# Performance work log

Measured on AMD Instinct MI355X. Metric: run time of the kernel, lower is better.

## Reference

```python
import jax, jax.numpy as jnp
import numpy as np

D = 256
B, S, N = 4, 512, 4


def setup_inputs() -> dict:
    key = jax.random.key(0)
    ks = jax.random.split(key, 24)
    d, dq = D, D // 4
    std = 0.02
    inp = {
        'x':   jax.random.normal(ks[0], (B, S, N, d), jnp.float32),
        'Wq':  jax.random.normal(ks[1], (d, d), jnp.float32) * std,
        'Wk':  jax.random.normal(ks[2], (d, d), jnp.float32) * std,
        'Wv':  jax.random.normal(ks[3], (d, d), jnp.float32) * std,
        'Wg1': jax.random.normal(ks[4], (d, d), jnp.float32) * std,
        'bg1': jnp.zeros((d,), jnp.float32),
        'Wg2': jax.random.normal(ks[5], (d, d), jnp.float32) * std,
        'bg2': jnp.zeros((d,), jnp.float32),
        'We1': jax.random.normal(ks[6], (d, dq), jnp.float32) * std,
        'be1': jnp.zeros((dq,), jnp.float32),
        'We2': jax.random.normal(ks[7], (dq, 1), jnp.float32) * std,
        'be2': jnp.zeros((1,), jnp.float32),
        'Wa1': jax.random.normal(ks[8], (d, dq), jnp.float32) * std,
        'ba1': jnp.zeros((dq,), jnp.float32),
        'Wa2': jax.random.normal(ks[9], (dq, 1), jnp.float32) * std,
        'ba2': jnp.zeros((1,), jnp.float32),
        'Wo':  jax.random.normal(ks[10], (d, d), jnp.float32) * std,
        'bo':  jnp.zeros((d,), jnp.float32),
        'gamma': jnp.ones((d,), jnp.float32),
        'beta':  jnp.zeros((d,), jnp.float32),
    }
    return inp


def reference(x, Wq, Wk, Wv, Wg1, bg1, Wg2, bg2, We1, be1, We2, be2,
              Wa1, ba1, Wa2, ba2, Wo, bo, gamma, beta):
    b, s, n, f = x.shape
    xf = x.reshape(b * n, s, f)  # matches torch .view on contiguous x
    residual = xf

    q = xf @ Wq                                    # [bn, s, d]
    k = xf @ Wk
    v = xf @ Wv
    v_hat = jax.nn.silu(v @ Wg1 + bg1) @ Wg2 + bg2  # value_generator
    eta = jax.nn.sigmoid(jax.nn.silu(xf @ We1 + be1) @ We2 + be2) * 0.1 + 0.01   # [bn, s, 1]
    alpha = jax.nn.sigmoid(jax.nn.silu(xf @ Wa1 + ba1) @ Wa2 + ba2) * 0.5 + 0.5  # [bn, s, 1]

    # F.normalize(k, dim=-1): eps = 1e-12
    kn = k / jnp.maximum(jnp.linalg.norm(k, axis=-1, keepdims=True), 1e-12)

    M0 = jnp.zeros((b * n, f, f), x.dtype)

    def step(M, inp):
        q_t, k_t, v_t, e_t, a_t = inp  # [bn,d],[bn,d],[bn,d],[bn,1],[bn,1]
        out_t = jnp.einsum('bij,bj->bi', M, q_t)
        Mk = jnp.einsum('bij,bj->bi', M, k_t)
        e = e_t[:, :, None]  # [bn,1,1]
        a = a_t[:, :, None]
        # delta rule: M <- a*M - e*(Mk k^T) + e*(v k^T)
        M_new = a * M + e * ((v_t - Mk)[:, :, None] * k_t[:, None, :])
        return M_new, out_t

    seq = (jnp.swapaxes(q, 0, 1), jnp.swapaxes(kn, 0, 1), jnp.swapaxes(v_hat, 0, 1),
           jnp.swapaxes(eta, 0, 1), jnp.swapaxes(alpha, 0, 1))
    M, outs = jax.lax.scan(step, M0, seq)
    out = jnp.swapaxes(outs, 0, 1)  # [bn, s, d]

    y = out @ Wo + bo + residual  # dropout is identity in eval/reference
    mu = jnp.mean(y, axis=-1, keepdims=True)
    var = jnp.var(y, axis=-1, keepdims=True)
    y = (y - mu) / jnp.sqrt(var + 1e-5) * gamma + beta
    return y.reshape(b, s, n, f), M
```

## Files before the change

### kernel.cpp

```cpp
#include <hip/hip_runtime.h>

#define F_ 256
#define S_ 512
#define NH_ 16
#define CCH 32
#define NCH (S_/CCH)
#define KSTR 264
#define KTSTR 36
#define TSTR 40
#define PSTR 17

typedef __attribute__((ext_vector_type(8))) short short8_t;
typedef __attribute__((ext_vector_type(4))) float f32x4;

__device__ __forceinline__ float sigmoid_f(float x) { return 1.0f / (1.0f + __expf(-x)); }

__device__ __forceinline__ ushort f2bf(float x) {
  uint u = __float_as_uint(x);
  u += 0x7FFFu + ((u >> 16) & 1u);
  return (ushort)(u >> 16);
}
__device__ __forceinline__ float bf2f(ushort u) {
  return __uint_as_float((uint)u << 16);
}

template<int CTRL>
__device__ __forceinline__ float dpp_add(float x) {
  int y = __builtin_amdgcn_update_dpp(0, __float_as_int(x), CTRL, 0xf, 0xf, true);
  return x + __int_as_float(y);
}
__device__ __forceinline__ float red8(float x) {
  x = dpp_add<0xB1>(x);
  x = dpp_add<0x4E>(x);
  x = dpp_add<0x141>(x);
  return x;
}

__global__ __launch_bounds__(256) void wconv_k(
    const float* __restrict__ Wq, const float* __restrict__ Wk,
    const float* __restrict__ Wv, const float* __restrict__ Wg1,
    const float* __restrict__ Wg2, const float* __restrict__ Wo,
    const float* __restrict__ We1, const float* __restrict__ Wa1,
    const float* __restrict__ be1, const float* __restrict__ ba1,
    const float* __restrict__ x,
    ushort* __restrict__ Wt, float* __restrict__ beas,
    ushort* __restrict__ xb)
{
  const int blk = blockIdx.x, tid = threadIdx.x;
  if (blk >= 105) {
    const size_t base = (size_t)(blk - 105) * 16384;
    #pragma unroll
    for (int p = 0; p < 16; ++p) {
      const size_t o = base + (size_t)(((p << 8) + tid) << 2);
      const float4 v = *(const float4*)&x[o];
      ushort4 h4;
      h4.x = f2bf(v.x); h4.y = f2bf(v.y); h4.z = f2bf(v.z); h4.w = f2bf(v.w);
      *(ushort4*)&xb[o] = h4;
    }
    return;
  }
  if (blk == 104) {
    if (tid < 64) beas[tid] = be1[tid];
    else if (tid < 128) beas[tid] = ba1[tid - 64];
    return;
  }
  __shared__ float tile[64][65];
  const float* src; int N, k0, n0; size_t dstbase;
  if (blk < 96) {
    const int w = blk >> 4, tl = blk & 15;
    const float* ws_[6] = {Wq, Wk, Wv, Wg1, Wg2, Wo};
    const size_t dstb[6] = {0, 65536, 131072, 229376, 294912, 360448};
    src = ws_[w]; N = 256;
    k0 = (tl >> 2) * 64; n0 = (tl & 3) * 64;
    dstbase = dstb[w];
  } else {
    const int w = (blk - 96) >> 2, tl = (blk - 96) & 3;
    src = w ? Wa1 : We1; N = 64;
    k0 = tl * 64; n0 = 0;
    dstbase = w ? 212992 : 196608;
  }
  #pragma unroll
  for (int p = 0; p < 4; ++p) {
    const int idx = (p << 8) + tid;
    const int r = idx >> 4, c4 = (idx & 15) << 2;
    if (c4 < N) {
      const float4 v = *(const float4*)&src[(size_t)(k0 + r) * N + n0 + c4];
      tile[r][c4 + 0] = v.x; tile[r][c4 + 1] = v.y;
      tile[r][c4 + 2] = v.z; tile[r][c4 + 3] = v.w;
    }
  }
  __syncthreads();
  #pragma unroll
  for (int p = 0; p < 4; ++p) {
    const int idx = (p << 8) + tid;
    const int nl = idx >> 4, kc = (idx & 15) << 2;
    if (nl < ((blk < 96) ? 64 : 64) && (n0 + nl) < ((blk < 96) ? 256 : 64)) {
      ushort4 o;
      o.x = f2bf(tile[kc + 0][nl]); o.y = f2bf(tile[kc + 1][nl]);
      o.z = f2bf(tile[kc + 2][nl]); o.w = f2bf(tile[kc + 3][nl]);
      *(ushort4*)&Wt[dstbase + (size_t)(n0 + nl) * 256 + k0 + kc] = o;
    }
  }
}

__global__ __launch_bounds__(256) void qkve_k(
    const ushort* __restrict__ A, const ushort* __restrict__ Wt,
    const float* __restrict__ beas,
    ushort* __restrict__ qb, float* __restrict__ kf,
    ushort* __restrict__ vb, float* __restrict__ sesa)
{
  __shared__ ushort As[2][64 * 72];
  __shared__ ushort Ws[2][64 * 72];
  const int tid = threadIdx.x;
  const int wv = tid >> 6, l = tid & 63;
  const int ln = l & 15, hi = l >> 4, hi4 = hi << 2, hi8 = hi << 3;
  const int wr = wv >> 1, wc = wv & 1;
  const int row0 = blockIdx.y * 64, col0 = blockIdx.x * 64;
  const int r_ = tid >> 3, c8_ = (tid & 7) << 3;

  short8_t pA[2], pB[2];
  auto loadT = [&](int k0) {
    pA[0] = *(const short8_t*)&A[(size_t)(row0 + r_) * 256 + k0 + c8_];
    pA[1] = *(const short8_t*)&A[(size_t)(row0 + 32 + r_) * 256 + k0 + c8_];
    pB[0] = *(const short8_t*)&Wt[(size_t)(col0 + r_) * 256 + k0 + c8_];
    pB[1] = *(const short8_t*)&Wt[(size_t)(col0 + 32 + r_) * 256 + k0 + c8_];
  };
  auto commitT = [&](int b) {
    *(short8_t*)&As[b][r_ * 72 + c8_] = pA[0];
    *(short8_t*)&As[b][(32 + r_) * 72 + c8_] = pA[1];
    *(short8_t*)&Ws[b][r_ * 72 + c8_] = pB[0];
    *(short8_t*)&Ws[b][(32 + r_) * 72 + c8_] = pB[1];
  };

  f32x4 acc[2][2];
  #pragma unroll
  for (int i = 0; i < 2; ++i)
    #pragma unroll
    for (int j = 0; j < 2; ++j)
      #pragma unroll
      for (int r = 0; r < 4; ++r) acc[i][j][r] = 0.f;

  loadT(0); commitT(0); __syncthreads();
  #pragma unroll
  for (int t = 0; t < 4; ++t) {
    const int b = t & 1;
    if (t < 3) loadT((t + 1) << 6);
    #pragma unroll
    for (int kk = 0; kk < 2; ++kk) {
      short8_t a0 = *(const short8_t*)&As[b][(wr * 32 + ln) * 72 + kk * 32 + hi8];
      short8_t a1 = *(const short8_t*)&As[b][(wr * 32 + 16 + ln) * 72 + kk * 32 + hi8];
      short8_t b0 = *(const short8_t*)&Ws[b][(wc * 32 + ln) * 72 + kk * 32 + hi8];
      short8_t b1 = *(const short8_t*)&Ws[b][(wc * 32 + 16 + ln) * 72 + kk * 32 + hi8];
      acc[0][0] = __builtin_amdgcn_mfma_f32_16x16x32_bf16(a0, b0, acc[0][0], 0, 0, 0);
      acc[0][1] = __builtin_amdgcn_mfma_f32_16x16x32_bf16(a0, b1, acc[0][1], 0, 0, 0);
      acc[1][0] = __builtin_amdgcn_mfma_f32_16x16x32_bf16(a1, b0, acc[1][0], 0, 0, 0);
      acc[1][1] = __builtin_amdgcn_mfma_f32_16x16x32_bf16(a1, b1, acc[1][1], 0, 0, 0);
    }
    if (t < 3) commitT(b ^ 1);
    __syncthreads();
  }

  #pragma unroll
  for (int mi = 0; mi < 2; ++mi)
    #pragma unroll
    for (int ni = 0; ni < 2; ++ni) {
      const int col = col0 + wc * 32 + ni * 16 + ln;
      #pragma unroll
      for (int r = 0; r < 4; ++r) {
        const int row = row0 + wr * 32 + mi * 16 + hi4 + r;
        float vx = acc[mi][ni][r];
        if (col0 < 256)      qb[(size_t)row * 256 + col] = f2bf(vx);
        else if (col0 < 512) kf[(size_t)row * 256 + (col - 256)] = vx;
        else if (col0 < 768) vb[(size_t)row * 256 + (col - 512)] = f2bf(vx);
        else {
          const int cc = col - 768;
          vx += beas[cc];
          vx *= sigmoid_f(vx);
          sesa[(size_t)row * 128 + cc] = vx;
        }
      }
    }
}

__global__ __launch_bounds__(256) void gemm_bf16_k(
    const ushort* __restrict__ A, const ushort* __restrict__ Wt,
    const float* __restrict__ bias, float* __restrict__ Cf,
    ushort* __restrict__ Cb, int act)
{
  __shared__ ushort As[2][64 * 72];
  __shared__ ushort Ws[2][64 * 72];
  const int tid = threadIdx.x;
  const int wv = tid >> 6, l = tid & 63;
  const int ln = l & 15, hi = l >> 4, hi4 = hi << 2, hi8 = hi << 3;
  const int wr = wv >> 1, wc = wv & 1;
  const int row0 = blockIdx.y * 64, col0 = blockIdx.x * 64;
  const int r_ = tid >> 3, c8_ = (tid & 7) << 3;

  short8_t pA[2], pB[2];
  auto loadT = [&](int k0) {
    pA[0] = *(const short8_t*)&A[(size_t)(row0 + r_) * 256 + k0 + c8_];
    pA[1] = *(const short8_t*)&A[(size_t)(row0 + 32 + r_) * 256 + k0 + c8_];
    pB[0] = *(const short8_t*)&Wt[(size_t)(col0 + r_) * 256 + k0 + c8_];
    pB[1] = *(const short8_t*)&Wt[(size_t)(col0 + 32 + r_) * 256 + k0 + c8_];
  };
  auto commitT = [&](int b) {
    *(short8_t*)&As[b][r_ * 72 + c8_] = pA[0];
    *(short8_t*)&As[b][(32 + r_) * 72 + c8_] = pA[1];
    *(short8_t*)&Ws[b][r_ * 72 + c8_] = pB[0];
    *(short8_t*)&Ws[b][(32 + r_) * 72 + c8_] = pB[1];
  };

  f32x4 acc[2][2];
  #pragma unroll
  for (int i = 0; i < 2; ++i)
    #pragma unroll
    for (int j = 0; j < 2; ++j)
      #pragma unroll
      for (int r = 0; r < 4; ++r) acc[i][j][r] = 0.f;

  loadT(0); commitT(0); __syncthreads();
  #pragma unroll
  for (int t = 0; t < 4; ++t) {
    const int b = t & 1;
    if (t < 3) loadT((t + 1) << 6);
    #pragma unroll
    for (int kk = 0; kk < 2; ++kk) {
      short8_t a0 = *(const short8_t*)&As[b][(wr * 32 + ln) * 72 + kk * 32 + hi8];
      short8_t a1 = *(const short8_t*)&As[b][(wr * 32 + 16 + ln) * 72 + kk * 32 + hi8];
      short8_t b0 = *(const short8_t*)&Ws[b][(wc * 32 + ln) * 72 + kk * 32 + hi8];
      short8_t b1 = *(const short8_t*)&Ws[b][(wc * 32 + 16 + ln) * 72 + kk * 32 + hi8];
      acc[0][0] = __builtin_amdgcn_mfma_f32_16x16x32_bf16(a0, b0, acc[0][0], 0, 0, 0);
      acc[0][1] = __builtin_amdgcn_mfma_f32_16x16x32_bf16(a0, b1, acc[0][1], 0, 0, 0);
      acc[1][0] = __builtin_amdgcn_mfma_f32_16x16x32_bf16(a1, b0, acc[1][0], 0, 0, 0);
      acc[1][1] = __builtin_amdgcn_mfma_f32_16x16x32_bf16(a1, b1, acc[1][1], 0, 0, 0);
    }
    if (t < 3) commitT(b ^ 1);
    __syncthreads();
  }

  #pragma unroll
  for (int mi = 0; mi < 2; ++mi)
    #pragma unroll
    for (int ni = 0; ni < 2; ++ni) {
      const int col = col0 + wc * 32 + ni * 16 + ln;
      const float bval = bias ? bias[col] : 0.f;
      #pragma unroll
      for (int r = 0; r < 4; ++r) {
        const int row = row0 + wr * 32 + mi * 16 + hi4 + r;
        float vx = acc[mi][ni][r] + bval;
        if (act == 1) vx = vx * sigmoid_f(vx);
        if (Cf) Cf[(size_t)row * 256 + col] = vx;
        if (Cb) Cb[(size_t)row * 256 + col] = f2bf(vx);
      }
    }
}

__global__ __launch_bounds__(256) void knea_k(
    const float* __restrict__ kf, ushort* __restrict__ kb,
    const float* __restrict__ sesa,
    const float* __restrict__ We2, const float* __restrict__ be2,
    const float* __restrict__ Wa2, const float* __restrict__ ba2,
    float* __restrict__ eta, float* __restrict__ alpha)
{
  const int lane = threadIdx.x & 63;
  const size_t row = ((size_t)blockIdx.x << 2) + (threadIdx.x >> 6);
  {
    const size_t off = row * F_ + ((size_t)lane << 2);
    float4 v = *(const float4*)&kf[off];
    float ss = v.x * v.x + v.y * v.y + v.z * v.z + v.w * v.w;
    #pragma unroll
    for (int m = 1; m < 64; m <<= 1) ss += __shfl_xor(ss, m, 64);
    const float sc = 1.0f / fmaxf(sqrtf(ss), 1e-12f);
    ushort4 o;
    o.x = f2bf(v.x * sc); o.y = f2bf(v.y * sc);
    o.z = f2bf(v.z * sc); o.w = f2bf(v.w * sc);
    *(ushort4*)&kb[off] = o;
  }
  {
    float pe = sesa[row * 128 + lane] * We2[lane];
    float pa = sesa[row * 128 + 64 + lane] * Wa2[lane];
    #pragma unroll
    for (int m = 1; m < 64; m <<= 1) {
      pe += __shfl_xor(pe, m, 64);
      pa += __shfl_xor(pa, m, 64);
    }
    if (lane == 0) {
      eta[row]   = sigmoid_f(pe + be2[0]) * 0.1f + 0.01f;
      alpha[row] = sigmoid_f(pa + ba2[0]) * 0.5f + 0.5f;
    }
  }
}

__global__ __launch_bounds__(256) void ln_k(
    const float* __restrict__ t, const float* __restrict__ x,
    const float* __restrict__ gamma, const float* __restrict__ beta,
    float* __restrict__ y)
{
  const int lane = threadIdx.x & 63;
  const size_t row = ((size_t)blockIdx.x << 2) + (threadIdx.x >> 6);
  const size_t off = row * F_ + ((size_t)lane << 2);
  const float4 tv = *(const float4*)&t[off];
  const float4 xv = *(const float4*)&x[off];
  float4 v = make_float4(tv.x + xv.x, tv.y + xv.y, tv.z + xv.z, tv.w + xv.w);
  float sm = v.x + v.y + v.z + v.w;
  float sq = v.x * v.x + v.y * v.y + v.z * v.z + v.w * v.w;
  #pragma unroll
  for (int m = 1; m < 64; m <<= 1) {
    sm += __shfl_xor(sm, m, 64);
    sq += __shfl_xor(sq, m, 64);
  }
  const float mu  = sm * (1.0f / 256.0f);
  const float var = sq * (1.0f / 256.0f) - mu * mu;
  const float rstd = rsqrtf(var + 1e-5f);
  const float4 g = *(const float4*)&gamma[(size_t)lane << 2];
  const float4 b = *(const float4*)&beta[(size_t)lane << 2];
  float4 o;
  o.x = (v.x - mu) * rstd * g.x + b.x;
  o.y = (v.y - mu) * rstd * g.y + b.y;
  o.z = (v.z - mu) * rstd * g.z + b.z;
  o.w = (v.w - mu) * rstd * g.w + b.w;
  *(float4*)&y[off] = o;
}

__global__ __launch_bounds__(256) void prep_k(
    const ushort* __restrict__ kb, const ushort* __restrict__ qb,
    const float* __restrict__ eta, const float* __restrict__ alpha,
    ushort* __restrict__ Tg, ushort* __restrict__ Gqg, float* __restrict__ Sg,
    ushort* __restrict__ Ktg)
{
  __shared__ ushort K_lds[CCH * KSTR];
  __shared__ ushort Q_lds[CCH * KSTR];
  __shared__ float  G_lds[CCH * CCH];
  __shared__ float  ea[2 * CCH];
  __shared__ float  scal[100];

  const int tid = threadIdx.x;
  const int ch = blockIdx.x, h = blockIdx.y;
  const int t0 = ch * CCH;
  const int l = tid & 63, wv = tid >> 6;
  const int ln = l & 15, hi = l >> 4;
  const int hi8 = hi * 8, hi4 = hi * 4;

  const ushort* kg = kb + (size_t)(h * S_ + t0) * F_;
  const ushort* qg = qb + (size_t)(h * S_ + t0) * F_;
  #pragma unroll
  for (int w = 0; w < 4; ++w) {
    int o = w * 256 + tid; int t = o >> 5, c8 = (o & 31) << 3;
    *(short8_t*)&K_lds[t * KSTR + c8] = *(const short8_t*)&kg[(size_t)t * F_ + c8];
    *(short8_t*)&Q_lds[t * KSTR + c8] = *(const short8_t*)&qg[(size_t)t * F_ + c8];
  }
  if (tid < CCH)            ea[tid] = eta[(size_t)h * S_ + t0 + tid];
  else if (tid < 2 * CCH)   ea[tid] = alpha[(size_t)h * S_ + t0 + tid - CCH];
  __syncthreads();

  {
    const int tt = tid & 31, cl = tid >> 5;
// ... 39 lines not shown
  __syncthreads();

  {
    const int j = tid >> 3, g = tid & 7;
    float x0 = 0.f, x1 = 0.f, x2 = 0.f, x3 = 0.f;
    ushort* To = Tg + (size_t)(h * NCH + ch) * (CCH * CCH);
    #pragma unroll
    for (int t = 0; t < CCH; ++t) {
      float p = 0.f;
      const f32x4 gr = *(const f32x4*)&G_lds[t * CCH + 4 * g];
      if (4 * g + 0 < t) p += gr[0] * x0;
      if (4 * g + 1 < t) p += gr[1] * x1;
      if (4 * g + 2 < t) p += gr[2] * x2;
      if (4 * g + 3 < t) p += gr[3] * x3;
      const float tot = red8(p);
      const float xt = ((t == j) ? 1.f : 0.f) - scal[t] * tot;
      if (g == (t >> 2)) {
        if ((t & 3) == 0) x0 = xt; else if ((t & 3) == 1) x1 = xt;
        else if ((t & 3) == 2) x2 = xt; else x3 = xt;
      }
      if (g == 0) To[t * CCH + j] = f2bf(xt);
    }
  }
  if (tid < 97) Sg[(size_t)(h * NCH + ch) * 128 + tid] = scal[tid];
}

__global__ __launch_bounds__(256, 1) void scan_chunk_k(
    const ushort* __restrict__ kb, const ushort* __restrict__ qb,
    const ushort* __restrict__ vhb, const ushort* __restrict__ Ktg,
    const ushort* __restrict__ Tg, const ushort* __restrict__ Gqg,
    const float* __restrict__ Sg,
    ushort* __restrict__ outb, float* __restrict__ Mout)
{
  __shared__ ushort K_lds[CCH * KSTR];
  __shared__ ushort Q_lds[CCH * KSTR];
  __shared__ ushort Kt_lds[2][F_ * KTSTR];
  __shared__ ushort M_lds[2][16 * KSTR];
  __shared__ ushort T_lds[CCH * TSTR];
  __shared__ ushort Gq_lds[2][CCH * TSTR];
  __shared__ ushort Wt_lds[16 * TSTR];
  __shared__ ushort R_lds[16 * TSTR];
  __shared__ float  KMp[4 * CCH * PSTR];
  __shared__ float  QM_lds[CCH * PSTR];
  __shared__ ushort V_lds[CCH * 16];
  __shared__ float  scal[2][104];

  const int tid = threadIdx.x;
  const int flat = blockIdx.x;
  const int h = (flat & 7) + ((flat >> 7) << 3);
  const int slice = (flat >> 3) & 15;
  const int r0 = slice * 16;
  const int wv = tid >> 6, l = tid & 63;
  const int ln = l & 15, hi = l >> 4, hi4 = hi << 2, hi8 = hi << 3;

  for (int u = tid; u < 16 * KSTR / 8; u += 256) {
    short8_t z = {0, 0, 0, 0, 0, 0, 0, 0};
    *(short8_t*)&M_lds[0][u * 8] = z;
  }
  f32x4 Mf[4];
  #pragma unroll
  for (int q = 0; q < 4; ++q)
    #pragma unroll
    for (int r = 0; r < 4; ++r) Mf[q][r] = 0.f;

  const ushort* kgh = kb + (size_t)h * S_ * F_;
  const ushort* qgh = qb + (size_t)h * S_ * F_;
  const ushort* kth = Ktg + (size_t)h * F_ * S_;

  short8_t pK[4], pQ[4], pKt[4], pTG;
  ushort pV[2]; float pS = 0.f;

  auto loadchunk = [&](int ch) {
    const int t0 = ch * CCH;
    #pragma unroll
    for (int r = 0; r < 4; ++r) {
      const int idx = (r << 8) + tid;
      const int t = idx >> 5, c8 = (idx & 31) << 3;
      pK[r] = *(const short8_t*)&kgh[(size_t)(t0 + t) * F_ + c8];
      pQ[r] = *(const short8_t*)&qgh[(size_t)(t0 + t) * F_ + c8];
    }
    #pragma unroll
    for (int r = 0; r < 4; ++r) {
      const int idx = (r << 8) + tid;
      const int c = idx >> 2, t8 = (idx & 3) << 3;
      pKt[r] = *(const short8_t*)&kth[(size_t)c * S_ + t0 + t8];
    }
    #pragma unroll
    for (int u = 0; u < 2; ++u) {
      const int e = (u << 8) + tid, t = e >> 4, i = e & 15;
      pV[u] = vhb[(size_t)(h * S_ + t0 + t) * F_ + r0 + i];
    }
    {
      const ushort* Ti = Tg  + (size_t)(h * NCH + ch) * (CCH * CCH);
      const ushort* Gi = Gqg + (size_t)(h * NCH + ch) * (CCH * CCH);
      if (tid < 128) {
        const int t = tid >> 2, c8 = (tid & 3) << 3;
        pTG = *(const short8_t*)&Ti[t * CCH + c8];
      } else {
        const int t = (tid - 128) >> 2, c8 = ((tid - 128) & 3) << 3;
        pTG = *(const short8_t*)&Gi[t * CCH + c8];
      }
    }
    if (tid < 97) pS = Sg[(size_t)(h * NCH + ch) * 128 + tid];
  };

  auto commit = [&](int b) {
    #pragma unroll
    for (int r = 0; r < 4; ++r) {
      const int idx = (r << 8) + tid;
      const int t = idx >> 5, c8 = (idx & 31) << 3;
      *(short8_t*)&K_lds[t * KSTR + c8] = pK[r];
      *(short8_t*)&Q_lds[t * KSTR + c8] = pQ[r];
    }
    #pragma unroll
    for (int r = 0; r < 4; ++r) {
      const int idx = (r << 8) + tid;
      const int c = idx >> 2, t8 = (idx & 3) << 3;
      *(short8_t*)&Kt_lds[b][c * KTSTR + t8] = pKt[r];
    }
    #pragma unroll
    for (int u = 0; u < 2; ++u) V_lds[(u << 8) + tid] = pV[u];
    if (tid < 128) {
      const int t = tid >> 2, c8 = (tid & 3) << 3;
      *(short8_t*)&T_lds[t * TSTR + c8] = pTG;
    } else {
      const int t = (tid - 128) >> 2, c8 = ((tid - 128) & 3) << 3;
      *(short8_t*)&Gq_lds[b][t * TSTR + c8] = pTG;
    }
    if (tid < 97) scal[b][tid] = pS;
  };

  loadchunk(0);
  commit(0);
  __syncthreads();
  int cb = 0;

  for (int ch = 0; ch < NCH; ++ch) {
    const int t0 = ch * CCH;
    const int nb = cb ^ 1;
    if (ch + 1 < NCH) loadchunk(ch + 1);

    {
      const int j0 = wv * 64;
      f32x4 a0v = {0.f, 0.f, 0.f, 0.f};
      f32x4 a1v = {0.f, 0.f, 0.f, 0.f};
      #pragma unroll
      for (int ks = 0; ks < 2; ++ks) {
        const int jc = j0 + ks * 32 + hi8;
        short8_t bm = *(const short8_t*)&M_lds[cb][ln * KSTR + jc];
        short8_t a0 = *(const short8_t*)&K_lds[ln * KSTR + jc];
        short8_t a1 = *(const short8_t*)&K_lds[(16 + ln) * KSTR + jc];
        a0v = __builtin_amdgcn_mfma_f32_16x16x32_bf16(a0, bm, a0v, 0, 0, 0);
        a1v = __builtin_amdgcn_mfma_f32_16x16x32_bf16(a1, bm, a1v, 0, 0, 0);
      }
      #pragma unroll
      for (int r = 0; r < 4; ++r) {
        KMp[wv * (CCH * PSTR) + (hi4 + r) * PSTR + ln] = a0v[r];
        KMp[wv * (CCH * PSTR) + (16 + hi4 + r) * PSTR + ln] = a1v[r];
      }
    }
    __syncthreads();

    if (wv == 0) {
      const int i = l & 15, tg = l >> 4;
      short8_t rv;
      #pragma unroll
      for (int u = 0; u < 8; ++u) {
        const int t = tg * 8 + u;
        const float s = KMp[t * PSTR + i]
                      + KMp[CCH * PSTR + t * PSTR + i]
                      + KMp[2 * CCH * PSTR + t * PSTR + i]
                      + KMp[3 * CCH * PSTR + t * PSTR + i];
        const float rhs = scal[cb][CCH + t] * bf2f(V_lds[t * 16 + i])
                        - scal[cb][t] * s;
        rv[u] = (short)f2bf(rhs);
      }
      *(short8_t*)&R_lds[i * TSTR + tg * 8] = rv;
      #pragma unroll
      for (int I = 0; I < 2; ++I) {
        short8_t a = *(const short8_t*)&T_lds[(I * 16 + ln) * TSTR + hi8];
        short8_t b = *(const short8_t*)&R_lds[ln * TSTR + hi8];
        f32x4 z = {0.f, 0.f, 0.f, 0.f};
        f32x4 d = __builtin_amdgcn_mfma_f32_16x16x32_bf16(a, b, z, 0, 0, 0);
        ushort4 wo;
        wo.x = f2bf(d[0]); wo.y = f2bf(d[1]); wo.z = f2bf(d[2]); wo.w = f2bf(d[3]);
        *(ushort4*)&Wt_lds[ln * TSTR + I * 16 + hi4] = wo;
      }
    } else if (wv >= 2) {
      const int I = wv - 2;
      f32x4 acc = {0.f, 0.f, 0.f, 0.f};
      #pragma unroll
      for (int ko = 0; ko < 8; ++ko) {
        short8_t a = *(const short8_t*)&Q_lds[(I * 16 + ln) * KSTR + ko * 32 + hi8];
        short8_t b = *(const short8_t*)&M_lds[cb][ln * KSTR + ko * 32 + hi8];
        acc = __builtin_amdgcn_mfma_f32_16x16x32_bf16(a, b, acc, 0, 0, 0);
      }
      #pragma unroll
      for (int r = 0; r < 4; ++r)
        QM_lds[(I * 16 + hi4 + r) * PSTR + ln] = acc[r];
    }
    __syncthreads();

    {
      const float gC = scal[cb][3 * CCH];
      short8_t aw = *(const short8_t*)&Wt_lds[ln * TSTR + hi8];
      #pragma unroll
      for (int qq = 0; qq < 4; ++qq) {
        const int jt = wv * 4 + qq;
        short8_t bk = *(const short8_t*)&Kt_lds[cb][(jt * 16 + ln) * KTSTR + hi8];
        f32x4 d = __builtin_amdgcn_mfma_f32_16x16x32_bf16(aw, bk, Mf[qq], 0, 0, 0);
        #pragma unroll
        for (int r = 0; r < 4; ++r) {
          const float nv = gC * d[r];
          Mf[qq][r] = nv;
          M_lds[nb][(hi4 + r) * KSTR + jt * 16 + ln] = f2bf(nv);
        }
      }
    }
    if (wv < 2) {
      const int I = wv;
      short8_t a = *(const short8_t*)&Gq_lds[cb][(I * 16 + ln) * TSTR + hi8];
      short8_t b = *(const short8_t*)&Wt_lds[ln * TSTR + hi8];
      f32x4 z = {0.f, 0.f, 0.f, 0.f};
      f32x4 d = __builtin_amdgcn_mfma_f32_16x16x32_bf16(a, b, z, 0, 0, 0);
      #pragma unroll
      for (int r = 0; r < 4; ++r) {
        const int t = I * 16 + hi4 + r;
        const float ov = scal[cb][2 * CCH + t] * (QM_lds[t * PSTR + ln] + d[r]);
        outb[(size_t)(h * S_ + t0 + t) * F_ + r0 + ln] = f2bf(ov);
      }
    }
    if (ch + 1 < NCH) commit(nb);
    __syncthreads();
    cb = nb;
  }

  #pragma unroll
  for (int qq = 0; qq < 4; ++qq) {
    const int jt = wv * 4 + qq;
    #pragma unroll
    for (int r = 0; r < 4; ++r)
      Mout[((size_t)h * F_ + r0 + hi4 + r) * F_ + jt * 16 + ln] = Mf[qq][r];
  }
}

extern "C" void kernel_launch(void* const* d_in, const int* in_sizes, int n_in,
                              void* d_out, int out_size, void* d_ws, size_t ws_size,
                              hipStream_t stream)
{
  const float* x    = (const float*)d_in[0];
  const float* Wq   = (const float*)d_in[1];
  const float* Wk   = (const float*)d_in[2];
  const float* Wv   = (const float*)d_in[3];
  const float* Wg1  = (const float*)d_in[4];
  const float* bg1  = (const float*)d_in[5];
  const float* Wg2  = (const float*)d_in[6];
  const float* bg2  = (const float*)d_in[7];
  const float* We1  = (const float*)d_in[8];
  const float* be1  = (const float*)d_in[9];
  const float* We2  = (const float*)d_in[10];
  const float* be2  = (const float*)d_in[11];
  const float* Wa1  = (const float*)d_in[12];
  const float* ba1  = (const float*)d_in[13];
  const float* Wa2  = (const float*)d_in[14];
  const float* ba2  = (const float*)d_in[15];
  const float* Wo   = (const float*)d_in[16];
  const float* bo   = (const float*)d_in[17];
  const float* gamma= (const float*)d_in[18];
  const float* beta = (const float*)d_in[19];

  const int Mrows = NH_ * S_;
  const size_t MM = 1048576;
  const size_t NTF = 2 * MM;

  float* ws = (float*)d_ws;
  ushort* xb   = (ushort*)(ws + 0 * MM);
  ushort* outb = (ushort*)(ws + 0 * MM);
  ushort* qb   = (ushort*)(ws + 1 * MM);
  ushort* kb   = (ushort*)(ws + 2 * MM);
  float*  kf   = ws + 3 * MM;
  ushort* t1b  = (ushort*)(ws + 3 * MM);
  ushort* vhb  = (ushort*)(ws + 4 * MM);
  ushort* vb   = (ushort*)(ws + 5 * MM);
  float*  sesa = ws + 6 * MM;
  float*  ytmp = ws + 5 * MM;
  float*  eta  = ws + 7 * MM;
  float*  alpha= eta + Mrows;
  ushort* Tg   = (ushort*)(ws + 7 * MM + 16384);
  ushort* Gqg  = Tg + 262144;
  float*  Sg   = ws + 7 * MM + 16384 + 131072 + 131072;
  ushort* Ktg  = (ushort*)(Sg + 32768);
  ushort* Wt   = Ktg + 2097152;
  float*  beas = (float*)(Wt + 425984);

  dim3 blk(256);

  wconv_k<<<233, blk, 0, stream>>>(Wq, Wk, Wv, Wg1, Wg2, Wo, We1, Wa1,
                                   be1, ba1, x, Wt, beas, xb);

  qkve_k<<<dim3(14, 128), blk, 0, stream>>>(xb, Wt, beas, qb, kf, vb, sesa);

  knea_k<<<Mrows / 4, blk, 0, stream>>>(kf, kb, sesa, We2, be2, Wa2, ba2, eta, alpha);

  gemm_bf16_k<<<dim3(4, 128), blk, 0, stream>>>(vb,  Wt + 229376, bg1, nullptr, t1b, 1);
  gemm_bf16_k<<<dim3(4, 128), blk, 0, stream>>>(t1b, Wt + 294912, bg2, nullptr, vhb, 0);

  prep_k<<<dim3(NCH, NH_), blk, 0, stream>>>(kb, qb, eta, alpha, Tg, Gqg, Sg, Ktg);

  float* yout = (float*)d_out;
  float* Mfin = yout + NTF;
  scan_chunk_k<<<256, blk, 0, stream>>>(kb, qb, vhb, Ktg, Tg, Gqg, Sg, outb, Mfin);

  gemm_bf16_k<<<dim3(4, 128), blk, 0, stream>>>(outb, Wt + 360448, bo, ytmp, nullptr, 0);
  ln_k<<<Mrows / 4, blk, 0, stream>>>(ytmp, x, gamma, beta, yout);
}
```

Baseline: 101.2 us.

## Fuse x bf16 conversion into QKV GEMM, fuse output GEMM with LayerNorm, restructure scan chunk

Removes the separate x-to-bf16 pass by having the QKV GEMM load fp32 x and convert while staging to LDS. Fuses the Wo GEMM with the residual add and LayerNorm into one kernel that owns full 256-column rows, which drops the fp32 ytmp round trip and the ln_k launch. The chunked scan kernel is reorganised: K/Q/T/V tiles are double-buffered, the KM product is split across two waves with k-split accumulators instead of four-way partials reduced in LDS, and M is kept in a single LDS buffer. This adds syncs per chunk and a larger LDS footprint in the fused LN kernel, which may lower occupancy with only 256 blocks.

Measured after the change: 100.1 us. About the same (-1.1%).

```diff
diff --git a/kernel.cpp b/kernel.cpp
--- a/kernel.cpp
+++ b/kernel.cpp
@@ -8,7 +8,6 @@
 #define KSTR 264
 #define KTSTR 36
 #define TSTR 40
-#define PSTR 17
 
 typedef __attribute__((ext_vector_type(8))) short short8_t;
 typedef __attribute__((ext_vector_type(4))) float f32x4;
@@ -42,23 +41,9 @@
     const float* __restrict__ Wg2, const float* __restrict__ Wo,
     const float* __restrict__ We1, const float* __restrict__ Wa1,
     const float* __restrict__ be1, const float* __restrict__ ba1,
-    const float* __restrict__ x,
-    ushort* __restrict__ Wt, float* __restrict__ beas,
-    ushort* __restrict__ xb)
+    ushort* __restrict__ Wt, float* __restrict__ beas)
 {
   const int blk = blockIdx.x, tid = threadIdx.x;
-  if (blk >= 105) {
-    const size_t base = (size_t)(blk - 105) * 16384;
-    #pragma unroll
-    for (int p = 0; p < 16; ++p) {
-      const size_t o = base + (size_t)(((p << 8) + tid) << 2);
-      const float4 v = *(const float4*)&x[o];
-      ushort4 h4;
-      h4.x = f2bf(v.x); h4.y = f2bf(v.y); h4.z = f2bf(v.z); h4.w = f2bf(v.w);
-      *(ushort4*)&xb[o] = h4;
-    }
-    return;
-  }
   if (blk == 104) {
     if (tid < 64) beas[tid] = be1[tid];
     else if (tid < 128) beas[tid] = ba1[tid - 64];
@@ -94,7 +79,7 @@
   for (int p = 0; p < 4; ++p) {
     const int idx = (p << 8) + tid;
     const int nl = idx >> 4, kc = (idx & 15) << 2;
-    if (nl < ((blk < 96) ? 64 : 64) && (n0 + nl) < ((blk < 96) ? 256 : 64)) {
+    if ((n0 + nl) < ((blk < 96) ? 256 : 64)) {
       ushort4 o;
       o.x = f2bf(tile[kc + 0][nl]); o.y = f2bf(tile[kc + 1][nl]);
       o.z = f2bf(tile[kc + 2][nl]); o.w = f2bf(tile[kc + 3][nl]);
@@ -104,10 +89,98 @@
 }
 
 __global__ __launch_bounds__(256) void qkve_k(
-    const ushort* __restrict__ A, const ushort* __restrict__ Wt,
+    const float* __restrict__ x, const ushort* __restrict__ Wt,
     const float* __restrict__ beas,
     ushort* __restrict__ qb, float* __restrict__ kf,
     ushort* __restrict__ vb, float* __restrict__ sesa)
+{
+  __shared__ ushort As[2][64 * 72];
+  __shared__ ushort Ws[2][64 * 72];
+  const int tid = threadIdx.x;
+  const int wv = tid >> 6, l = tid & 63;
+  const int ln = l & 15, hi = l >> 4, hi4 = hi << 2, hi8 = hi << 3;
+  const int wr = wv >> 1, wc = wv & 1;
+  const int row0 = blockIdx.y * 64, col0 = blockIdx.x * 64;
+  const int r_ = tid >> 3, c8_ = (tid & 7) << 3;
+
+  float4 pAf[4];
+  short8_t pB[2];
+  auto loadT = [&](int k0) {
+    pAf[0] = *(const float4*)&x[(size_t)(row0 + r_) * 256 + k0 + c8_];
+    pAf[1] = *(const float4*)&x[(size_t)(row0 + r_) * 256 + k0 + c8_ + 4];
+    pAf[2] = *(const float4*)&x[(size_t)(row0 + 32 + r_) * 256 + k0 + c8_];
+    pAf[3] = *(const float4*)&x[(size_t)(row0 + 32 + r_) * 256 + k0 + c8_ + 4];
+    pB[0] = *(const short8_t*)&Wt[(size_t)(col0 + r_) * 256 + k0 + c8_];
+    pB[1] = *(const short8_t*)&Wt[(size_t)(col0 + 32 + r_) * 256 + k0 + c8_];
+  };
+  auto commitT = [&](int b) {
+    #pragma unroll
+    for (int h = 0; h < 2; ++h) {
+      short8_t s;
+      s[0] = (short)f2bf(pAf[h*2].x); s[1] = (short)f2bf(pAf[h*2].y);
+      s[2] = (short)f2bf(pAf[h*2].z); s[3] = (short)f2bf(pAf[h*2].w);
+      s[4] = (short)f2bf(pAf[h*2+1].x); s[5] = (short)f2bf(pAf[h*2+1].y);
+      s[6] = (short)f2bf(pAf[h*2+1].z); s[7] = (short)f2bf(pAf[h*2+1].w);
+      *(short8_t*)&As[b][(h * 32 + r_) * 72 + c8_] = s;
+    }
+    *(short8_t*)&Ws[b][r_ * 72 + c8_] = pB[0];
+    *(short8_t*)&Ws[b][(32 + r_) * 72 + c8_] = pB[1];
+  };
+
+  f32x4 acc[2][2];
+  #pragma unroll
+  for (int i = 0; i < 2; ++i)
+    #pragma unroll
+    for (int j = 0; j < 2; ++j)
+      #pragma unroll
+      for (int r = 0; r < 4; ++r) acc[i][j][r] = 0.f;
+
+  loadT(0); commitT(0); __syncthreads();
+  #pragma unroll
+  for (int t = 0; t < 4; ++t) {
+    const int b = t & 1;
+    if (t < 3) loadT((t + 1) << 6);
+    #pragma unroll
+    for (int kk = 0; kk < 2; ++kk) {
+      short8_t a0 = *(const short8_t*)&As[b][(wr * 32 + ln) * 72 + kk * 32 + hi8];
+      short8_t a1 = *(const short8_t*)&As[b][(wr * 32 + 16 + ln) * 72 + kk * 32 + hi8];
+      short8_t b0 = *(const short8_t*)&Ws[b][(wc * 32 + ln) * 72 + kk * 32 + hi8];
+      short8_t b1 = *(const short8_t*)&Ws[b][(wc * 32 + 16 + ln) * 72 + kk * 32 + hi8];
+      acc[0][0] = __builtin_amdgcn_mfma_f32_16x16x32_bf16(a0, b0, acc[0][0], 0, 0, 0);
+      acc[0][1] = __builtin_amdgcn_mfma_f32_16x16x32_bf16(a0, b1, acc[0][1], 0, 0, 0);
+      acc[1][0] = __builtin_amdgcn_mfma_f32_16x16x32_bf16(a1, b0, acc[1][0], 0, 0, 0);
+      acc[1][1] = __builtin_amdgcn_mfma_f32_16x16x32_bf16(a1, b1, acc[1][1], 0, 0, 0);
+    }
+    if (t < 3) commitT(b ^ 1);
+    __syncthreads();
+  }
+
+  #pragma unroll
+  for (int mi = 0; mi < 2; ++mi)
+    #pragma unroll
+    for (int ni = 0; ni < 2; ++ni) {
+      const int col = col0 + wc * 32 + ni * 16 + ln;
+      #pragma unroll
+      for (int r = 0; r < 4; ++r) {
+        const int row = row0 + wr * 32 + mi * 16 + hi4 + r;
+        float vx = acc[mi][ni][r];
+        if (col0 < 256)      qb[(size_t)row * 256 + col] = f2bf(vx);
+        else if (col0 < 512) kf[(size_t)row * 256 + (col - 256)] = vx;
+        else if (col0 < 768) vb[(size_t)row * 256 + (col - 512)] = f2bf(vx);
+        else {
+          const int cc = col - 768;
+          vx += beas[cc];
+          vx *= sigmoid_f(vx);
+          sesa[(size_t)row * 128 + cc] = vx;
+        }
+      }
+    }
+}
+
+__global__ __launch_bounds__(256) void gemm_bf16_k(
+    const ushort* __restrict__ A, const ushort* __restrict__ Wt,
+    const float* __restrict__ bias, float* __restrict__ Cf,
+    ushort* __restrict__ Cb, int act)
 {
   __shared__ ushort As[2][64 * 72];
   __shared__ ushort Ws[2][64 * 72];
@@ -165,84 +238,6 @@
     #pragma unroll
     for (int ni = 0; ni < 2; ++ni) {
       const int col = col0 + wc * 32 + ni * 16 + ln;
-      #pragma unroll
-      for (int r = 0; r < 4; ++r) {
-        const int row = row0 + wr * 32 + mi * 16 + hi4 + r;
-        float vx = acc[mi][ni][r];
-        if (col0 < 256)      qb[(size_t)row * 256 + col] = f2bf(vx);
-        else if (col0 < 512) kf[(size_t)row * 256 + (col - 256)] = vx;
-        else if (col0 < 768) vb[(size_t)row * 256 + (col - 512)] = f2bf(vx);
-        else {
-          const int cc = col - 768;
-          vx += beas[cc];
-          vx *= sigmoid_f(vx);
-          sesa[(size_t)row * 128 + cc] = vx;
-        }
-      }
-    }
-}
-
-__global__ __launch_bounds__(256) void gemm_bf16_k(
-    const ushort* __restrict__ A, const ushort* __restrict__ Wt,
-    const float* __restrict__ bias, float* __restrict__ Cf,
-    ushort* __restrict__ Cb, int act)
-{
-  __shared__ ushort As[2][64 * 72];
-  __shared__ ushort Ws[2][64 * 72];
-  const int tid = threadIdx.x;
-  const int wv = tid >> 6, l = tid & 63;
-  const int ln = l & 15, hi = l >> 4, hi4 = hi << 2, hi8 = hi << 3;
-  const int wr = wv >> 1, wc = wv & 1;
-  const int row0 = blockIdx.y * 64, col0 = blockIdx.x * 64;
-  const int r_ = tid >> 3, c8_ = (tid & 7) << 3;
-
-  short8_t pA[2], pB[2];
-  auto loadT = [&](int k0) {
-    pA[0] = *(const short8_t*)&A[(size_t)(row0 + r_) * 256 + k0 + c8_];
-    pA[1] = *(const short8_t*)&A[(size_t)(row0 + 32 + r_) * 256 + k0 + c8_];
-    pB[0] = *(const short8_t*)&Wt[(size_t)(col0 + r_) * 256 + k0 + c8_];
-    pB[1] = *(const short8_t*)&Wt[(size_t)(col0 + 32 + r_) * 256 + k0 + c8_];
-  };
-  auto commitT = [&](int b) {
-    *(short8_t*)&As[b][r_ * 72 + c8_] = pA[0];
-    *(short8_t*)&As[b][(32 + r_) * 72 + c8_] = pA[1];
-    *(short8_t*)&Ws[b][r_ * 72 + c8_] = pB[0];
-    *(short8_t*)&Ws[b][(32 + r_) * 72 + c8_] = pB[1];
-  };
-
-  f32x4 acc[2][2];
-  #pragma unroll
-  for (int i = 0; i < 2; ++i)
-    #pragma unroll
-    for (int j = 0; j < 2; ++j)
-      #pragma unroll
-      for (int r = 0; r < 4; ++r) acc[i][j][r] = 0.f;
-
-  loadT(0); commitT(0); __syncthreads();
-  #pragma unroll
-  for (int t = 0; t < 4; ++t) {
-    const int b = t & 1;
-    if (t < 3) loadT((t + 1) << 6);
-    #pragma unroll
-    for (int kk = 0; kk < 2; ++kk) {
-      short8_t a0 = *(const short8_t*)&As[b][(wr * 32 + ln) * 72 + kk * 32 + hi8];
-      short8_t a1 = *(const short8_t*)&As[b][(wr * 32 + 16 + ln) * 72 + kk * 32 + hi8];
-      short8_t b0 = *(const short8_t*)&Ws[b][(wc * 32 + ln) * 72 + kk * 32 + hi8];
-      short8_t b1 = *(const short8_t*)&Ws[b][(wc * 32 + 16 + ln) * 72 + kk * 32 + hi8];
-      acc[0][0] = __builtin_amdgcn_mfma_f32_16x16x32_bf16(a0, b0, acc[0][0], 0, 0, 0);
-      acc[0][1] = __builtin_amdgcn_mfma_f32_16x16x32_bf16(a0, b1, acc[0][1], 0, 0, 0);
-      acc[1][0] = __builtin_amdgcn_mfma_f32_16x16x32_bf16(a1, b0, acc[1][0], 0, 0, 0);
-      acc[1][1] = __builtin_amdgcn_mfma_f32_16x16x32_bf16(a1, b1, acc[1][1], 0, 0, 0);
-    }
-    if (t < 3) commitT(b ^ 1);
-    __syncthreads();
-  }
-
-  #pragma unroll
-  for (int mi = 0; mi < 2; ++mi)
-    #pragma unroll
-    for (int ni = 0; ni < 2; ++ni) {
-      const int col = col0 + wc * 32 + ni * 16 + ln;
       const float bval = bias ? bias[col] : 0.f;
       #pragma unroll
       for (int r = 0; r < 4; ++r) {
@@ -253,6 +248,116 @@
         if (Cb) Cb[(size_t)row * 256 + col] = f2bf(vx);
       }
     }
+}
+
+__global__ __launch_bounds__(256) void gemmo_ln_k(
+    const ushort* __restrict__ A, const ushort* __restrict__ Wt,
+    const float* __restrict__ bo, const float* __restrict__ x,
+    const float* __restrict__ gamma, const float* __restrict__ beta,
+    float* __restrict__ y)
+{
+  __shared__ ushort As[2][32 * 72];
+  __shared__ ushort Ws[2][256 * 72];
+  __shared__ float rs_[2][32];
+  __shared__ float rq_[2][32];
+  const int tid = threadIdx.x;
+  const int wv = tid >> 6, l = tid & 63;
+  const int ln = l & 15, hi = l >> 4, hi4 = hi << 2, hi8 = hi << 3;
+  const int g = wv >> 1, chf = wv & 1;
+  const int row0 = blockIdx.x * 32;
+
+  short8_t pA, pW[8];
+  auto loadT = [&](int k0) {
+    { const int r = tid >> 3, c8 = (tid & 7) << 3;
+      pA = *(const short8_t*)&A[(size_t)(row0 + r) * 256 + k0 + c8]; }
+    #pragma unroll
+    for (int p = 0; p < 8; ++p) {
+      const int idx = (p << 8) + tid;
+      const int n = idx >> 3, c8 = (idx & 7) << 3;
+      pW[p] = *(const short8_t*)&Wt[(size_t)n * 256 + k0 + c8];
+    }
+  };
+  auto commitT = [&](int b) {
+    { const int r = tid >> 3, c8 = (tid & 7) << 3;
+      *(short8_t*)&As[b][r * 72 + c8] = pA; }
+    #pragma unroll
+    for (int p = 0; p < 8; ++p) {
+      const int idx = (p << 8) + tid;
+      const int n = idx >> 3, c8 = (idx & 7) << 3;
+      *(short8_t*)&Ws[b][n * 72 + c8] = pW[p];
+    }
+  };
+
+  f32x4 acc[8];
+  #pragma unroll
+  for (int nt = 0; nt < 8; ++nt)
+    #pragma unroll
+    for (int r = 0; r < 4; ++r) acc[nt][r] = 0.f;
+
+  loadT(0); commitT(0); __syncthreads();
+  #pragma unroll
+  for (int t = 0; t < 4; ++t) {
+    const int b = t & 1;
+    if (t < 3) loadT((t + 1) << 6);
+    #pragma unroll
+    for (int kk = 0; kk < 2; ++kk) {
+      short8_t a = *(const short8_t*)&As[b][(g * 16 + ln) * 72 + kk * 32 + hi8];
+      #pragma unroll
+      for (int nt = 0; nt < 8; ++nt) {
+        short8_t bb = *(const short8_t*)&Ws[b][(chf * 128 + nt * 16 + ln) * 72 + kk * 32 + hi8];
+        acc[nt] = __builtin_amdgcn_mfma_f32_16x16x32_bf16(a, bb, acc[nt], 0, 0, 0);
+      }
+    }
+    if (t < 3) commitT(b ^ 1);
+    __syncthreads();
+  }
+
+  float val[8][4];
+  float sm[4] = {0.f, 0.f, 0.f, 0.f}, sq[4] = {0.f, 0.f, 0.f, 0.f};
+  #pragma unroll
+  for (int nt = 0; nt < 8; ++nt) {
+    const int col = chf * 128 + nt * 16 + ln;
+    const float bv = bo[col];
+    #pragma unroll
+    for (int r = 0; r < 4; ++r) {
+      const int row = row0 + g * 16 + hi4 + r;
+      const float v = acc[nt][r] + bv + x[(size_t)row * 256 + col];
+      val[nt][r] = v;
+      sm[r] += v;
+      sq[r] += v * v;
+    }
+  }
+  #pragma unroll
+  for (int m = 1; m < 16; m <<= 1) {
+    #pragma unroll
+    for (int r = 0; r < 4; ++r) {
+      sm[r] += __shfl_xor(sm[r], m, 64);
+      sq[r] += __shfl_xor(sq[r], m, 64);
+    }
+  }
+  if (ln == 0) {
+    #pragma unroll
+    for (int r = 0; r < 4; ++r) {
+      rs_[chf][g * 16 + hi4 + r] = sm[r];
+      rq_[chf][g * 16 + hi4 + r] = sq[r];
+    }
+  }
+  __syncthreads();
+  #pragma unroll
+  for (int r = 0; r < 4; ++r) {
+    const int lr = g * 16 + hi4 + r;
+    const float tot = rs_[0][lr] + rs_[1][lr];
+    const float tq  = rq_[0][lr] + rq_[1][lr];
+    const float mu  = tot * (1.0f / 256.0f);
+    const float var = tq * (1.0f / 256.0f) - mu * mu;
+    const float rstd = rsqrtf(var + 1e-5f);
+    #pragma unroll
+    for (int nt = 0; nt < 8; ++nt) {
+      const int col = chf * 128 + nt * 16 + ln;
+      y[(size_t)(row0 + lr) * 256 + col] =
+          (val[nt][r] - mu) * rstd * gamma[col] + beta[col];
+    }
+  }
 }
 
 __global__ __launch_bounds__(256) void knea_k(
@@ -291,37 +396,6 @@
   }
 }
 
-__global__ __launch_bounds__(256) void ln_k(
-    const float* __restrict__ t, const float* __restrict__ x,
-    const float* __restrict__ gamma, const float* __restrict__ beta,
-    float* __restrict__ y)
-{
-  const int lane = threadIdx.x & 63;
-  const size_t row = ((size_t)blockIdx.x << 2) + (threadIdx.x >> 6);
-  const size_t off = row * F_ + ((size_t)lane << 2);
-  const float4 tv = *(const float4*)&t[off];
-  const float4 xv = *(const float4*)&x[off];
-  float4 v = make_float4(tv.x + xv.x, tv.y + xv.y, tv.z + xv.z, tv.w + xv.w);
-  float sm = v.x + v.y + v.z + v.w;
-  float sq = v.x * v.x + v.y * v.y + v.z * v.z + v.w * v.w;
-  #pragma unroll
-  for (int m = 1; m < 64; m <<= 1) {
-    sm += __shfl_xor(sm, m, 64);
-    sq += __shfl_xor(sq, m, 64);
-  }
-  const float mu  = sm * (1.0f / 256.0f);
-  const float var = sq * (1.0f / 256.0f) - mu * mu;
-  const float rstd = rsqrtf(var + 1e-5f);
-  const float4 g = *(const float4*)&gamma[(size_t)lane << 2];
-  const float4 b = *(const float4*)&beta[(size_t)lane << 2];
-  float4 o;
-  o.x = (v.x - mu) * rstd * g.x + b.x;
-  o.y = (v.y - mu) * rstd * g.y + b.y;
-  o.z = (v.z - mu) * rstd * g.z + b.z;
-  o.w = (v.w - mu) * rstd * g.w + b.w;
-  *(float4*)&y[off] = o;
-}
-
 __global__ __launch_bounds__(256) void prep_k(
     const ushort* __restrict__ kb, const ushort* __restrict__ qb,
     const float* __restrict__ eta, const float* __restrict__ alpha,
@@ -427,22 +501,21 @@
     const float* __restrict__ Sg,
     ushort* __restrict__ outb, float* __restrict__ Mout)
 {
-  __shared__ ushort K_lds[CCH * KSTR];
-  __shared__ ushort Q_lds[CCH * KSTR];
+  __shared__ ushort K_lds[2][CCH * KSTR];
+  __shared__ ushort Q_lds[2][CCH * KSTR];
   __shared__ ushort Kt_lds[2][F_ * KTSTR];
-  __shared__ ushort M_lds[2][16 * KSTR];
-  __shared__ ushort T_lds[CCH * TSTR];
+  __shared__ ushort M_lds[16 * KSTR];
+  __shared__ ushort T_lds[2][CCH * TSTR];
   __shared__ ushort Gq_lds[2][CCH * TSTR];
   __shared__ ushort Wt_lds[16 * TSTR];
   __shared__ ushort R_lds[16 * TSTR];
-  __shared__ float  KMp[4 * CCH * PSTR];
-  __shared__ float  QM_lds[CCH * PSTR];
-  __shared__ ushort V_lds[CCH * 16];
+  __shared__ float  QM_lds[CCH * 20];
+  __shared__ ushort V_lds[2][CCH * 16];
   __shared__ float  scal[2][104];
 
   const int tid = threadIdx.x;
   const int flat = blockIdx.x;
-  const int h = (flat & 7) + ((flat >> 7) << 3);
+  const int h = (flat & 7) + (((flat >> 3) >> 4) << 3);
   const int slice = (flat >> 3) & 15;
   const int r0 = slice * 16;
   const int wv = tid >> 6, l = tid & 63;
@@ -450,7 +523,7 @@
 
   for (int u = tid; u < 16 * KSTR / 8; u += 256) {
     short8_t z = {0, 0, 0, 0, 0, 0, 0, 0};
-    *(short8_t*)&M_lds[0][u * 8] = z;
+    *(short8_t*)&M_lds[u * 8] = z;
   }
   f32x4 Mf[4];
   #pragma unroll
@@ -499,135 +572,130 @@
     if (tid < 97) pS = Sg[(size_t)(h * NCH + ch) * 128 + tid];
   };
 
-  auto commit = [&](int b) {
+  auto commit = [&](int buf) {
     #pragma unroll
     for (int r = 0; r < 4; ++r) {
       const int idx = (r << 8) + tid;
       const int t = idx >> 5, c8 = (idx & 31) << 3;
-      *(short8_t*)&K_lds[t * KSTR + c8] = pK[r];
-      *(short8_t*)&Q_lds[t * KSTR + c8] = pQ[r];
+      *(short8_t*)&K_lds[buf][t * KSTR + c8] = pK[r];
+      *(short8_t*)&Q_lds[buf][t * KSTR + c8] = pQ[r];
     }
     #pragma unroll
     for (int r = 0; r < 4; ++r) {
       const int idx = (r << 8) + tid;
       const int c = idx >> 2, t8 = (idx & 3) << 3;
-      *(short8_t*)&Kt_lds[b][c * KTSTR + t8] = pKt[r];
-    }
-    #pragma unroll
-    for (int u = 0; u < 2; ++u) V_lds[(u << 8) + tid] = pV[u];
+      *(short8_t*)&Kt_lds[buf][c * KTSTR + t8] = pKt[r];
+    }
+    #pragma unroll
+    for (int u = 0; u < 2; ++u) V_lds[buf][(u << 8) + tid] = pV[u];
     if (tid < 128) {
       const int t = tid >> 2, c8 = (tid & 3) << 3;
-      *(short8_t*)&T_lds[t * TSTR + c8] = pTG;
+      *(short8_t*)&T_lds[buf][t * TSTR + c8] = pTG;
     } else {
       const int t = (tid - 128) >> 2, c8 = ((tid - 128) & 3) << 3;
-      *(short8_t*)&Gq_lds[b][t * TSTR + c8] = pTG;
-    }
-    if (tid < 97) scal[b][tid] = pS;
+      *(short8_t*)&Gq_lds[buf][t * TSTR + c8] = pTG;
+    }
+    if (tid < 97) scal[buf][tid] = pS;
   };
 
   loadchunk(0);
   commit(0);
   __syncthreads();
-  int cb = 0;
 
   for (int ch = 0; ch < NCH; ++ch) {
+    const int buf = ch & 1;
     const int t0 = ch * CCH;
-    const int nb = cb ^ 1;
     if (ch + 1 < NCH) loadchunk(ch + 1);
 
+    if (wv < 2) {
+      const int I = wv;
+      f32x4 a0 = {0.f, 0.f, 0.f, 0.f}, a1 = {0.f, 0.f, 0.f, 0.f};
+      #pragma unroll
+      for (int ko = 0; ko < 4; ++ko) {
+        {
+          short8_t a = *(const short8_t*)&K_lds[buf][(I * 16 + ln) * KSTR + (2 * ko) * 32 + hi8];
+          short8_t b = *(const short8_t*)&M_lds[ln * KSTR + (2 * ko) * 32 + hi8];
+          a0 = __builtin_amdgcn_mfma_f32_16x16x32_bf16(a, b, a0, 0, 0, 0);
+        }
+        {
+          short8_t a = *(const short8_t*)&K_lds[buf][(I * 16 + ln) * KSTR + (2 * ko + 1) * 32 + hi8];
+          short8_t b = *(const short8_t*)&M_lds[ln * KSTR + (2 * ko + 1) * 32 + hi8];
+          a1 = __builtin_amdgcn_mfma_f32_16x16x32_bf16(a, b, a1, 0, 0, 0);
+        }
+      }
+      #pragma unroll
+      for (int r = 0; r < 4; ++r) {
+        const int t = I * 16 + hi4 + r;
+        const float s = a0[r] + a1[r];
+        const float rhs = scal[buf][CCH + t] * bf2f(V_lds[buf][t * 16 + ln])
+                        - scal[buf][t] * s;
+        R_lds[ln * TSTR + t] = f2bf(rhs);
+      }
+    } else {
+      const int I = wv - 2;
+      f32x4 a0 = {0.f, 0.f, 0.f, 0.f}, a1 = {0.f, 0.f, 0.f, 0.f};
+      #pragma unroll
+      for (int ko = 0; ko < 4; ++ko) {
+        {
+          short8_t a = *(const short8_t*)&Q_lds[buf][(I * 16 + ln) * KSTR + (2 * ko) * 32 + hi8];
+          short8_t b = *(const short8_t*)&M_lds[ln * KSTR + (2 * ko) * 32 + hi8];
+          a0 = __builtin_amdgcn_mfma_f32_16x16x32_bf16(a, b, a0, 0, 0, 0);
+        }
+        {
+          short8_t a = *(const short8_t*)&Q_lds[buf][(I * 16 + ln) * KSTR + (2 * ko + 1) * 32 + hi8];
+          short8_t b = *(const short8_t*)&M_lds[ln * KSTR + (2 * ko + 1) * 32 + hi8];
+          a1 = __builtin_amdgcn_mfma_f32_16x16x32_bf16(a, b, a1, 0, 0, 0);
+        }
+      }
+      #pragma unroll
+      for (int r = 0; r < 4; ++r)
+        QM_lds[(I * 16 + hi4 + r) * 20 + ln] = a0[r] + a1[r];
+    }
+    __syncthreads();
+
+    if (wv < 2) {
+      const int I = wv;
+      short8_t a = *(const short8_t*)&T_lds[buf][(I * 16 + ln) * TSTR + hi8];
+      short8_t b = *(const short8_t*)&R_lds[ln * TSTR + hi8];
+      f32x4 z = {0.f, 0.f, 0.f, 0.f};
+      f32x4 d = __builtin_amdgcn_mfma_f32_16x16x32_bf16(a, b, z, 0, 0, 0);
+      #pragma unroll
+      for (int r = 0; r < 4; ++r)
+        Wt_lds[ln * TSTR + I * 16 + hi4 + r] = f2bf(d[r]);
+    }
+    __syncthreads();
+
+    if (wv < 2) {
+      const int I = wv;
+      short8_t a = *(const short8_t*)&Gq_lds[buf][(I * 16 + ln) * TSTR + hi8];
+      short8_t b = *(const short8_t*)&Wt_lds[ln * TSTR + hi8];
+      f32x4 z = {0.f, 0.f, 0.f, 0.f};
+      f32x4 d = __builtin_amdgcn_mfma_f32_16x16x32_bf16(a, b, z, 0, 0, 0);
+      #pragma unroll
+      for (int r = 0; r < 4; ++r) {
+        const int t = I * 16 + hi4 + r;
+        outb[(size_t)(h * S_ + t0 + t) * F_ + r0 + ln] =
+            f2bf(scal[buf][2 * CCH + t] * (QM_lds[t * 20 + ln] + d[r]));
+      }
+    }
     {
-      const int j0 = wv * 64;
-      f32x4 a0v = {0.f, 0.f, 0.f, 0.f};
-      f32x4 a1v = {0.f, 0.f, 0.f, 0.f};
-      #pragma unroll
-      for (int ks = 0; ks < 2; ++ks) {
-        const int jc = j0 + ks * 32 + hi8;
-        short8_t bm = *(const short8_t*)&M_lds[cb][ln * KSTR + jc];
-        short8_t a0 = *(const short8_t*)&K_lds[ln * KSTR + jc];
-        short8_t a1 = *(const short8_t*)&K_lds[(16 + ln) * KSTR + jc];
-        a0v = __builtin_amdgcn_mfma_f32_16x16x32_bf16(a0, bm, a0v, 0, 0, 0);
-        a1v = __builtin_amdgcn_mfma_f32_16x16x32_bf16(a1, bm, a1v, 0, 0, 0);
-      }
-      #pragma unroll
-      for (int r = 0; r < 4; ++r) {
-        KMp[wv * (CCH * PSTR) + (hi4 + r) * PSTR + ln] = a0v[r];
-        KMp[wv * (CCH * PSTR) + (16 + hi4 + r) * PSTR + ln] = a1v[r];
-      }
-    }
-    __syncthreads();
-
-    if (wv == 0) {
-      const int i = l & 15, tg = l >> 4;
-      short8_t rv;
-      #pragma unroll
-      for (int u = 0; u < 8; ++u) {
-        const int t = tg * 8 + u;
-        const float s = KMp[t * PSTR + i]
-                      + KMp[CCH * PSTR + t * PSTR + i]
-                      + KMp[2 * CCH * PSTR + t * PSTR + i]
-                      + KMp[3 * CCH * PSTR + t * PSTR + i];
-        const float rhs = scal[cb][CCH + t] * bf2f(V_lds[t * 16 + i])
-                        - scal[cb][t] * s;
-        rv[u] = (short)f2bf(rhs);
-      }
-      *(short8_t*)&R_lds[i * TSTR + tg * 8] = rv;
-      #pragma unroll
-      for (int I = 0; I < 2; ++I) {
-        short8_t a = *(const short8_t*)&T_lds[(I * 16 + ln) * TSTR + hi8];
-        short8_t b = *(const short8_t*)&R_lds[ln * TSTR + hi8];
-        f32x4 z = {0.f, 0.f, 0.f, 0.f};
-        f32x4 d = __builtin_amdgcn_mfma_f32_16x16x32_bf16(a, b, z, 0, 0, 0);
-        ushort4 wo;
-        wo.x = f2bf(d[0]); wo.y = f2bf(d[1]); wo.z = f2bf(d[2]); wo.w = f2bf(d[3]);
-        *(ushort4*)&Wt_lds[ln * TSTR + I * 16 + hi4] = wo;
-      }
-    } else if (wv >= 2) {
-      const int I = wv - 2;
-      f32x4 acc = {0.f, 0.f, 0.f, 0.f};
-      #pragma unroll
-      for (int ko = 0; ko < 8; ++ko) {
-        short8_t a = *(const short8_t*)&Q_lds[(I * 16 + ln) * KSTR + ko * 32 + hi8];
-        short8_t b = *(const short8_t*)&M_lds[cb][ln * KSTR + ko * 32 + hi8];
-        acc = __builtin_amdgcn_mfma_f32_16x16x32_bf16(a, b, acc, 0, 0, 0);
-      }
-      #pragma unroll
-      for (int r = 0; r < 4; ++r)
-        QM_lds[(I * 16 + hi4 + r) * PSTR + ln] = acc[r];
-    }
-    __syncthreads();
-
-    {
-      const float gC = scal[cb][3 * CCH];
+      const float gC = scal[buf][3 * CCH];
       short8_t aw = *(const short8_t*)&Wt_lds[ln * TSTR + hi8];
       #pragma unroll
       for (int qq = 0; qq < 4; ++qq) {
         const int jt = wv * 4 + qq;
-        short8_t bk = *(const short8_t*)&Kt_lds[cb][(jt * 16 + ln) * KTSTR + hi8];
+        short8_t bk = *(const short8_t*)&Kt_lds[buf][(jt * 16 + ln) * KTSTR + hi8];
         f32x4 d = __builtin_amdgcn_mfma_f32_16x16x32_bf16(aw, bk, Mf[qq], 0, 0, 0);
         #pragma unroll
         for (int r = 0; r < 4; ++r) {
           const float nv = gC * d[r];
           Mf[qq][r] = nv;
-          M_lds[nb][(hi4 + r) * KSTR + jt * 16 + ln] = f2bf(nv);
+          M_lds[(hi4 + r) * KSTR + jt * 16 + ln] = f2bf(nv);
         }
       }
     }
-    if (wv < 2) {
-      const int I = wv;
-      short8_t a = *(const short8_t*)&Gq_lds[cb][(I * 16 + ln) * TSTR + hi8];
-      short8_t b = *(const short8_t*)&Wt_lds[ln * TSTR + hi8];
-      f32x4 z = {0.f, 0.f, 0.f, 0.f};
-      f32x4 d = __builtin_amdgcn_mfma_f32_16x16x32_bf16(a, b, z, 0, 0, 0);
-      #pragma unroll
-      for (int r = 0; r < 4; ++r) {
-        const int t = I * 16 + hi4 + r;
-        const float ov = scal[cb][2 * CCH + t] * (QM_lds[t * PSTR + ln] + d[r]);
-        outb[(size_t)(h * S_ + t0 + t) * F_ + r0 + ln] = f2bf(ov);
-      }
-    }
-    if (ch + 1 < NCH) commit(nb);
+    if (ch + 1 < NCH) commit(buf ^ 1);
     __syncthreads();
-    cb = nb;
   }
 
   #pragma unroll
@@ -669,7 +737,6 @@
   const size_t NTF = 2 * MM;
 
   float* ws = (float*)d_ws;
-  ushort* xb   = (ushort*)(ws + 0 * MM);
   ushort* outb = (ushort*)(ws + 0 * MM);
   ushort* qb   = (ushort*)(ws + 1 * MM);
   ushort* kb   = (ushort*)(ws + 2 * MM);
@@ -678,7 +745,6 @@
   ushort* vhb  = (ushort*)(ws + 4 * MM);
   ushort* vb   = (ushort*)(ws + 5 * MM);
   float*  sesa = ws + 6 * MM;
-  float*  ytmp = ws + 5 * MM;
   float*  eta  = ws + 7 * MM;
   float*  alpha= eta + Mrows;
   ushort* Tg   = (ushort*)(ws + 7 * MM + 16384);
@@ -690,10 +756,10 @@
 
   dim3 blk(256);
 
-  wconv_k<<<233, blk, 0, stream>>>(Wq, Wk, Wv, Wg1, Wg2, Wo, We1, Wa1,
-                                   be1, ba1, x, Wt, beas, xb);
-
-  qkve_k<<<dim3(14, 128), blk, 0, stream>>>(xb, Wt, beas, qb, kf, vb, sesa);
+  wconv_k<<<105, blk, 0, stream>>>(Wq, Wk, Wv, Wg1, Wg2, Wo, We1, Wa1,
+                                   be1, ba1, Wt, beas);
+
+  qkve_k<<<dim3(14, 128), blk, 0, stream>>>(x, Wt, beas, qb, kf, vb, sesa);
 
   knea_k<<<Mrows / 4, blk, 0, stream>>>(kf, kb, sesa, We2, be2, Wa2, ba2, eta, alpha);
 
@@ -706,6 +772,5 @@
   float* Mfin = yout + NTF;
   scan_chunk_k<<<256, blk, 0, stream>>>(kb, qb, vhb, Ktg, Tg, Gqg, Sg, outb, Mfin);
 
-  gemm_bf16_k<<<dim3(4, 128), blk, 0, stream>>>(outb, Wt + 360448, bo, ytmp, nullptr, 0);
-  ln_k<<<Mrows / 4, blk, 0, stream>>>(ytmp, x, gamma, beta, yout);
-}
+  gemmo_ln_k<<<256, blk, 0, stream>>>(outb, Wt + 360448, bo, x, gamma, beta, yout);
+}
```
